# Kernel optimization log

Hardware: AMD Instinct MI355X
Metric: run time of the kernel (lower is better)

The kernel has to match this reference:

```python
import jax, jax.numpy as jnp
import numpy as np

B, N_LINKS, N_JOINTS, C_L, C_J = 4096, 33, 32, 64, 128

def setup_inputs() -> dict:
    key = jax.random.key(0)
    k1, k2, k3, k4 = jax.random.split(key, 4)
    link_feats = jax.random.normal(k1, (B, N_LINKS, C_L, 16), dtype=jnp.float32)
    joint_feats = jax.random.normal(k2, (B, N_JOINTS, C_J), dtype=jnp.float32)
    # Stacked per-joint Linear weights: [J, C_L*16, C_J], bias [J, C_J]
    fan_in = C_L * 16
    W = jax.random.normal(k3, (N_JOINTS, fan_in, C_J), dtype=jnp.float32) / np.sqrt(fan_in).astype(np.float32)
    b = jax.random.normal(k4, (N_JOINTS, C_J), dtype=jnp.float32) * 0.01
    child_idx = jnp.arange(1, N_JOINTS + 1, dtype=jnp.int64)  # child link of joint j is link j+1
    return {"link_feats": link_feats, "joint_feats": joint_feats, "W": W, "b": b, "child_idx": child_idx}

def reference(link_feats, joint_feats, W, b, child_idx):
    # Gather child-link features per joint: [B, J, C_L, 16] -> flatten to [B, J, C_L*16]
    Bsz = link_feats.shape[0]
    J = child_idx.shape[0]
    x = link_feats[:, child_idx].reshape(Bsz, J, -1)
    # Grouped GEMM over joints (replaces Python loop of tiny Linears), + bias + residual
    return jnp.einsum('bji,jio->bjo', x, W) + b[None, :, :] + joint_feats
```

## Files before the change

### kernel.cpp

```cpp
#include <hip/hip_runtime.h>
#include <hip/hip_bf16.h>

typedef __attribute__((ext_vector_type(8))) short bf16x8;
typedef __attribute__((ext_vector_type(4))) float f32x4;

#define NB    4096
#define NLINK 33
#define NJ    32
#define KTOT  1024
#define CJ    128
#define BM    128
#define BK    64

static __device__ __forceinline__ short f2bf(float f) {
    unsigned u = __builtin_bit_cast(unsigned, f);
    unsigned r = u + 0x7FFFu + ((u >> 16) & 1u);
    return (short)(r >> 16);
}

__global__ __launch_bounds__(256, 2) void joint_gemm(
    const float* __restrict__ link,
    const float* __restrict__ jf,
    const float* __restrict__ W,
    const float* __restrict__ bias,
    const int*   __restrict__ child,
    float* __restrict__ out)
{
    __shared__ bf16x8 lA[BK / 8][BM];
    __shared__ bf16x8 lB[BK / 8][CJ];

    const int tid  = threadIdx.x;
    const int lane = tid & 63;
    const int wave = tid >> 6;
    const int wr   = wave >> 1;
    const int wc   = wave & 1;

    const int bx = blockIdx.x;
    const int j  = bx & 31;
    const int mt = bx >> 5;
    const int rowbase = mt * BM;

    const int cidx = child[j];

    const int am   = tid >> 3;
    const int aks  = tid & 7;
    const int bn   = tid & 127;
    const int bks0 = tid >> 7;

    const float* Wj = W + (size_t)j * KTOT * CJ;

    f32x4 acc[4][4] = {};

    float4 fa[4][2];
    float  fb[4][8];

    auto load_tile = [&](int k0) {
        #pragma unroll
        for (int p = 0; p < 4; ++p) {
            const int m = p * 32 + am;
            const float* ar = link + ((size_t)(rowbase + m) * NLINK + cidx) * KTOT + k0 + aks * 8;
            const float4* a4 = reinterpret_cast<const float4*>(ar);
            fa[p][0] = a4[0];
            fa[p][1] = a4[1];
            const float* br = Wj + (size_t)(k0 + (bks0 + p * 2) * 8) * CJ + bn;
            #pragma unroll
            for (int e = 0; e < 8; ++e) fb[p][e] = br[(size_t)e * CJ];
        }
    };

    load_tile(0);

    for (int t = 0; t < KTOT / BK; ++t) {
        __syncthreads();
        #pragma unroll
        for (int p = 0; p < 4; ++p) {
            const float* fsrc = reinterpret_cast<const float*>(&fa[p][0]);
            bf16x8 va, vb;
            #pragma unroll
            for (int e = 0; e < 8; ++e) va[e] = f2bf(fsrc[e]);
            lA[aks][p * 32 + am] = va;
            #pragma unroll
            for (int e = 0; e < 8; ++e) vb[e] = f2bf(fb[p][e]);
            lB[bks0 + p * 2][bn] = vb;
        }
        __syncthreads();

        if (t + 1 < KTOT / BK) load_tile((t + 1) * BK);

        const int q = lane >> 4;
        const int r = lane & 15;
        #pragma unroll
        for (int kk = 0; kk < 2; ++kk) {
            bf16x8 af[4], bfr[4];
            #pragma unroll
            for (int mi = 0; mi < 4; ++mi) af[mi]  = lA[kk * 4 + q][wr * 64 + mi * 16 + r];
            #pragma unroll
            for (int ni = 0; ni < 4; ++ni) bfr[ni] = lB[kk * 4 + q][wc * 64 + ni * 16 + r];
            #pragma unroll
            for (int mi = 0; mi < 4; ++mi)
                #pragma unroll
                for (int ni = 0; ni < 4; ++ni)
                    acc[mi][ni] = __builtin_amdgcn_mfma_f32_16x16x32_bf16(
                        af[mi], bfr[ni], acc[mi][ni], 0, 0, 0);
        }
    }

    const int q = lane >> 4;
    const int r = lane & 15;
    float bv[4];
    #pragma unroll
    for (int ni = 0; ni < 4; ++ni) bv[ni] = bias[j * CJ + wc * 64 + ni * 16 + r];

    #pragma unroll
    for (int mi = 0; mi < 4; ++mi) {
        #pragma unroll
        for (int rr = 0; rr < 4; ++rr) {
            const int bg = rowbase + wr * 64 + mi * 16 + q * 4 + rr;
            const size_t obase = ((size_t)bg * NJ + j) * CJ;
            #pragma unroll
            for (int ni = 0; ni < 4; ++ni) {
                const int o = wc * 64 + ni * 16 + r;
                out[obase + o] = acc[mi][ni][rr] + bv[ni] + jf[obase + o];
            }
        }
    }
}

extern "C" void kernel_launch(void* const* d_in, const int* in_sizes, int n_in,
                              void* d_out, int out_size, void* d_ws, size_t ws_size,
                              hipStream_t stream) {
    (void)in_sizes; (void)n_in; (void)out_size; (void)d_ws; (void)ws_size;
    const float* link  = (const float*)d_in[0];
    const float* jfeat = (const float*)d_in[1];
    const float* W     = (const float*)d_in[2];
    const float* bias  = (const float*)d_in[3];
    const int*   child = (const int*)d_in[4];
    float* out = (float*)d_out;

    dim3 grid(NJ * (NB / BM));
    dim3 block(256);
    joint_gemm<<<grid, block, 0, stream>>>(link, jfeat, W, bias, child, out);
}
```

Baseline: 169.6 us.

## Pre-convert weights to bf16 fragment layout and double-buffer swizzled A tiles

A separate kernel converts W to bf16 once per call, packed in MFMA fragment order into a global buffer. The GEMM then loads B fragments straight from global memory into registers instead of staging them through LDS. A is double-buffered in LDS with an XOR swizzle, which keeps one barrier per K step and avoids bank conflicts. Blocks grow to 512 threads, so each wave computes a 32x64 tile. The cost is an extra kernel launch plus a 4 MB bf16 weight pass each call, and every wave re-reads B from cache.

```diff
diff --git a/kernel.cpp b/kernel.cpp
--- a/kernel.cpp
+++ b/kernel.cpp
@@ -11,6 +11,9 @@
 #define CJ    128
 #define BM    128
 #define BK    64
+#define NT    (KTOT / BK)
+
+__device__ short g_Wf[NJ * KTOT * CJ];
 
 static __device__ __forceinline__ short f2bf(float f) {
     unsigned u = __builtin_bit_cast(unsigned, f);
@@ -18,109 +21,125 @@
     return (short)(r >> 16);
 }
 
-__global__ __launch_bounds__(256, 2) void joint_gemm(
+__global__ __launch_bounds__(256) void conv_w(const float* __restrict__ W) {
+    const int gid = blockIdx.x * 256 + threadIdx.x;
+    const int q  = gid & 3;
+    const int c  = (gid >> 2) & 127;
+    const int kt = (gid >> 9) & 31;
+    const int j  = gid >> 14;
+    const float* src = W + ((size_t)j * KTOT + kt * 32 + q * 8) * CJ + c;
+    bf16x8 v;
+    #pragma unroll
+    for (int e = 0; e < 8; ++e) v[e] = f2bf(src[(size_t)e * CJ]);
+    reinterpret_cast<bf16x8*>(g_Wf)[gid] = v;
+}
+
+__global__ __launch_bounds__(512, 4) void joint_gemm(
     const float* __restrict__ link,
     const float* __restrict__ jf,
-    const float* __restrict__ W,
     const float* __restrict__ bias,
     const int*   __restrict__ child,
     float* __restrict__ out)
 {
-    __shared__ bf16x8 lA[BK / 8][BM];
-    __shared__ bf16x8 lB[BK / 8][CJ];
+    __shared__ short lA[2][BM * BK];
 
     const int tid  = threadIdx.x;
     const int lane = tid & 63;
     const int wave = tid >> 6;
     const int wr   = wave >> 1;
     const int wc   = wave & 1;
+    const int q    = lane >> 4;
+    const int r    = lane & 15;
+    const int xr   = r & 7;
 
     const int bx = blockIdx.x;
     const int j  = bx & 31;
     const int mt = bx >> 5;
     const int rowbase = mt * BM;
-
     const int cidx = child[j];
 
-    const int am   = tid >> 3;
-    const int aks  = tid & 7;
-    const int bn   = tid & 127;
-    const int bks0 = tid >> 7;
+    const int srow   = tid >> 2;
+    const int squart = tid & 3;
+    const float* abase = link + ((size_t)(rowbase + srow) * NLINK + cidx) * KTOT + squart * 16;
+    const int xw = srow & 7;
+    const int p0 = (squart * 2) ^ xw;
+    const int p1 = p0 ^ 1;
 
-    const float* Wj = W + (size_t)j * KTOT * CJ;
+    const bf16x8* wb = reinterpret_cast<const bf16x8*>(g_Wf);
+    const size_t bbase = ((size_t)j * 32 * 128 + wc * 64 + r) * 4 + q;
 
-    f32x4 acc[4][4] = {};
+    f32x4  acc[2][4] = {};
+    float4 fa4[4];
+    bf16x8 Breg[2][4];
 
-    float4 fa[4][2];
-    float  fb[4][8];
-
-    auto load_tile = [&](int k0) {
+    auto loadA = [&](int t) {
+        const float4* p = reinterpret_cast<const float4*>(abase + (size_t)t * BK);
+        fa4[0] = p[0]; fa4[1] = p[1]; fa4[2] = p[2]; fa4[3] = p[3];
+    };
+    auto stageA = [&](int b) {
+        const float* f = reinterpret_cast<const float*>(fa4);
+        bf16x8 v0, v1;
         #pragma unroll
-        for (int p = 0; p < 4; ++p) {
-            const int m = p * 32 + am;
-            const float* ar = link + ((size_t)(rowbase + m) * NLINK + cidx) * KTOT + k0 + aks * 8;
-            const float4* a4 = reinterpret_cast<const float4*>(ar);
-            fa[p][0] = a4[0];
-            fa[p][1] = a4[1];
-            const float* br = Wj + (size_t)(k0 + (bks0 + p * 2) * 8) * CJ + bn;
+        for (int e = 0; e < 8; ++e) { v0[e] = f2bf(f[e]); v1[e] = f2bf(f[8 + e]); }
+        bf16x8* Lw = reinterpret_cast<bf16x8*>(lA[b]) + srow * 8;
+        Lw[p0] = v0;
+        Lw[p1] = v1;
+    };
+    auto loadB = [&](int t) {
+        #pragma unroll
+        for (int kk = 0; kk < 2; ++kk)
             #pragma unroll
-            for (int e = 0; e < 8; ++e) fb[p][e] = br[(size_t)e * CJ];
-        }
+            for (int ni = 0; ni < 4; ++ni)
+                Breg[kk][ni] = wb[bbase + (size_t)(t * 2 + kk) * 512 + ni * 64];
     };
 
-    load_tile(0);
+    loadA(0);
+    loadB(0);
+    stageA(0);
+    loadA(1);
+    __syncthreads();
 
-    for (int t = 0; t < KTOT / BK; ++t) {
-        __syncthreads();
-        #pragma unroll
-        for (int p = 0; p < 4; ++p) {
-            const float* fsrc = reinterpret_cast<const float*>(&fa[p][0]);
-            bf16x8 va, vb;
-            #pragma unroll
-            for (int e = 0; e < 8; ++e) va[e] = f2bf(fsrc[e]);
-            lA[aks][p * 32 + am] = va;
-            #pragma unroll
-            for (int e = 0; e < 8; ++e) vb[e] = f2bf(fb[p][e]);
-            lB[bks0 + p * 2][bn] = vb;
-        }
-        __syncthreads();
+    int cur = 0;
+    for (int t = 0; t < NT; ++t) {
+        if (t + 1 < NT) stageA(cur ^ 1);
+        if (t + 2 < NT) loadA(t + 2);
 
-        if (t + 1 < KTOT / BK) load_tile((t + 1) * BK);
-
-        const int q = lane >> 4;
-        const int r = lane & 15;
+        const bf16x8* Lr = reinterpret_cast<const bf16x8*>(lA[cur]);
         #pragma unroll
         for (int kk = 0; kk < 2; ++kk) {
-            bf16x8 af[4], bfr[4];
+            bf16x8 af[2];
             #pragma unroll
-            for (int mi = 0; mi < 4; ++mi) af[mi]  = lA[kk * 4 + q][wr * 64 + mi * 16 + r];
+            for (int mi = 0; mi < 2; ++mi) {
+                const int R = wr * 32 + mi * 16 + r;
+                af[mi] = Lr[R * 8 + (((kk << 2) | q) ^ xr)];
+            }
             #pragma unroll
-            for (int ni = 0; ni < 4; ++ni) bfr[ni] = lB[kk * 4 + q][wc * 64 + ni * 16 + r];
-            #pragma unroll
-            for (int mi = 0; mi < 4; ++mi)
+            for (int mi = 0; mi < 2; ++mi)
                 #pragma unroll
                 for (int ni = 0; ni < 4; ++ni)
                     acc[mi][ni] = __builtin_amdgcn_mfma_f32_16x16x32_bf16(
-                        af[mi], bfr[ni], acc[mi][ni], 0, 0, 0);
+                        af[mi], Breg[kk][ni], acc[mi][ni], 0, 0, 0);
         }
+
+        if (t + 1 < NT) loadB(t + 1);
+        __syncthreads();
+        cur ^= 1;
     }
 
-    const int q = lane >> 4;
-    const int r = lane & 15;
     float bv[4];
     #pragma unroll
     for (int ni = 0; ni < 4; ++ni) bv[ni] = bias[j * CJ + wc * 64 + ni * 16 + r];
 
     #pragma unroll
-    for (int mi = 0; mi < 4; ++mi) {
+    for (int mi = 0; mi < 2; ++mi) {
         #pragma unroll
         for (int rr = 0; rr < 4; ++rr) {
-            const int bg = rowbase + wr * 64 + mi * 16 + q * 4 + rr;
-            const size_t obase = ((size_t)bg * NJ + j) * CJ;
+            const int bg = rowbase + wr * 32 + mi * 16 + q * 4 + rr;
+            const size_t ob = ((size_t)bg * NJ + j) * CJ;
             #pragma unroll
             for (int ni = 0; ni < 4; ++ni) {
                 const int o = wc * 64 + ni * 16 + r;
-                out[obase + o] = acc[mi][ni][rr] + bv[ni] + jf[obase + o];
+                out[ob + o] = acc[mi][ni][rr] + bv[ni] + jf[ob + o];
             }
         }
     }
@@ -137,7 +156,6 @@
     const int*   child = (const int*)d_in[4];
     float* out = (float*)d_out;
 
-    dim3 grid(NJ * (NB / BM));
-    dim3 block(256);
-    joint_gemm<<<grid, block, 0, stream>>>(link, jfeat, W, bias, child, out);
+    conv_w<<<dim3((NJ * KTOT * CJ / 8) / 256), dim3(256), 0, stream>>>(W);
+    joint_gemm<<<dim3(NJ * (NB / BM)), dim3(512), 0, stream>>>(link, jfeat, bias, child, out);
 }
```

Result: slower. 182.3 us (+7.5%).
